# Kernel optimization log

Hardware: AMD Instinct MI355X
Metric: run time of the kernel (lower is better)

The kernel has to match this reference:

```python
import jax, jax.numpy as jnp
import numpy as np

B, L, C = 64, 2688, 256
W, S, H = 42, 21, 8   # window_size, shift_size, num_heads
HD = C // H
NW = L // W
MLP_H = 4 * C


def _layer_norm(v, g, b, eps=1e-5):
    m = v.mean(-1, keepdims=True)
    var = ((v - m) ** 2).mean(-1, keepdims=True)
    return (v - m) / jnp.sqrt(var + eps) * g + b


def setup_inputs() -> dict:
    key = jax.random.key(0)
    ks = jax.random.split(key, 8)
    std = 0.02
    return {
        "x": jax.random.normal(ks[0], (B, L, C), jnp.float32),
        "norm1_g": jnp.ones((C,), jnp.float32),
        "norm1_b": jnp.zeros((C,), jnp.float32),
        "qkv_w": jax.random.normal(ks[1], (C, 3 * C), jnp.float32) * std,
        "qkv_b": jnp.zeros((3 * C,), jnp.float32),
        "bias_table": jax.random.normal(ks[2], (2 * W - 1, H), jnp.float32) * std,
        "proj_w": jax.random.normal(ks[3], (C, C), jnp.float32) * std,
        "proj_b": jnp.zeros((C,), jnp.float32),
        "norm2_g": jnp.ones((C,), jnp.float32),
        "norm2_b": jnp.zeros((C,), jnp.float32),
        "fc1_w": jax.random.normal(ks[4], (C, MLP_H), jnp.float32) * std,
        "fc1_b": jnp.zeros((MLP_H,), jnp.float32),
        "fc2_w": jax.random.normal(ks[5], (MLP_H, C), jnp.float32) * std,
        "fc2_b": jnp.zeros((C,), jnp.float32),
    }


# ---- static (data-independent) index/mask tables ----
_rel_idx = np.arange(W)[None, :] - np.arange(W)[:, None] + W - 1  # (W, W)
_seg = np.zeros((L,), np.float32)
_seg[-W:-S] = 1.0
_seg[-S:] = 2.0
_mw = _seg.reshape(NW, W)
_am = _mw[:, None, :] - _mw[:, :, None]            # (nW, W, W)
_ATTN_MASK = np.where(_am != 0, -100.0, 0.0).astype(np.float32)


def reference(x, norm1_g, norm1_b, qkv_w, qkv_b, bias_table, proj_w, proj_b,
              norm2_g, norm2_b, fc1_w, fc1_b, fc2_w, fc2_b):
    mask = jnp.asarray(_ATTN_MASK)                  # (nW, W, W)
    scale = HD ** -0.5

    shortcut = x
    h = _layer_norm(x, norm1_g, norm1_b)
    h = jnp.roll(h, -S, axis=1)                     # cyclic shift
    xw = h.reshape(B * NW, W, C)                    # window partition

    qkv = (xw @ qkv_w + qkv_b).reshape(B * NW, W, 3, H, HD).transpose(2, 0, 3, 1, 4)
    q, k, v = qkv[0] * scale, qkv[1], qkv[2]        # each (B_, H, W, HD)
    attn = jnp.einsum('bhnd,bhmd->bhnm', q, k)      # (B_, H, W, W)

    rpb = bias_table[jnp.asarray(_rel_idx)]         # (W, W, H)
    attn = attn + rpb.transpose(2, 0, 1)[None]
    attn = attn.reshape(B, NW, H, W, W) + mask[None, :, None]
    attn = jax.nn.softmax(attn.reshape(B * NW, H, W, W), axis=-1)

    o = jnp.einsum('bhnm,bhmd->bhnd', attn, v)      # (B_, H, W, HD)
    o = o.transpose(0, 2, 1, 3).reshape(B * NW, W, C)
    o = o @ proj_w + proj_b

    h = jnp.roll(o.reshape(B, L, C), S, axis=1)     # reverse shift
    x1 = shortcut + h

    m = _layer_norm(x1, norm2_g, norm2_b)
    m = jax.nn.gelu(m @ fc1_w + fc1_b, approximate=False)
    m = m @ fc2_w + fc2_b
    return x1 + m
```

## Files before the change

### kernel.cpp

```cpp
#include <hip/hip_runtime.h>
#include <hip/hip_bf16.h>

typedef short short8 __attribute__((ext_vector_type(8)));
typedef float floatx4 __attribute__((ext_vector_type(4)));

constexpr int Bc = 64, Lc = 2688, Cc = 256, Wc = 42, Sc = 21;
constexpr int Mrows = Bc * Lc;
constexpr float QSCALE = 0.17677669529663689f;

#define GLOAD_LDS(g, l) __builtin_amdgcn_global_load_lds( \
    (const __attribute__((address_space(1))) void*)(g),   \
    (__attribute__((address_space(3))) void*)(l), 16, 0, 0)
#define BAR() __builtin_amdgcn_s_barrier()
#define WAITV4() asm volatile("s_waitcnt vmcnt(4)" ::: "memory")
#define WAITV0() asm volatile("s_waitcnt vmcnt(0)" ::: "memory")
#define LGKM0() do { asm volatile("s_waitcnt lgkmcnt(0)" ::: "memory"); \
                     __builtin_amdgcn_sched_barrier(0); } while (0)

__global__ __launch_bounds__(256) void transpose_cast_k(const float* __restrict__ w,
                                                        __hip_bfloat16* __restrict__ o,
                                                        int K, int N) {
  __shared__ float tile[32][33];
  int tx = threadIdx.x & 31, ty = threadIdx.x >> 5;
  int n0 = blockIdx.x * 32, k0 = blockIdx.y * 32;
#pragma unroll
  for (int r = 0; r < 32; r += 8)
    tile[ty + r][tx] = w[(size_t)(k0 + ty + r) * N + n0 + tx];
  __syncthreads();
#pragma unroll
  for (int r = 0; r < 32; r += 8)
    o[(size_t)(n0 + ty + r) * K + k0 + tx] = __float2bfloat16(tile[tx][ty + r]);
}

__global__ __launch_bounds__(256) void ln_k(const float* __restrict__ x, const float* __restrict__ g,
                                            const float* __restrict__ bta, __hip_bfloat16* __restrict__ out,
                                            int roll) {
  int row = blockIdx.x * 4 + (threadIdx.x >> 6);
  int lane = threadIdx.x & 63;
  int bb = row / Lc, rl = row - bb * Lc;
  int sl = rl + roll; if (sl >= Lc) sl -= Lc;
  const float4 v = *(const float4*)(x + ((size_t)bb * Lc + sl) * Cc + lane * 4);
  float s = v.x + v.y + v.z + v.w;
#pragma unroll
  for (int o = 1; o < 64; o <<= 1) s += __shfl_xor(s, o, 64);
  float mean = s * (1.0f / Cc);
  float d0 = v.x - mean, d1 = v.y - mean, d2 = v.z - mean, d3 = v.w - mean;
  float s2 = d0 * d0 + d1 * d1 + d2 * d2 + d3 * d3;
#pragma unroll
  for (int o = 1; o < 64; o <<= 1) s2 += __shfl_xor(s2, o, 64);
  float r = rsqrtf(s2 * (1.0f / Cc) + 1e-5f);
  const float4 gg = *(const float4*)(g + lane * 4);
  const float4 bb4 = *(const float4*)(bta + lane * 4);
  __hip_bfloat16 tmp[4];
  tmp[0] = __float2bfloat16(d0 * r * gg.x + bb4.x);
  tmp[1] = __float2bfloat16(d1 * r * gg.y + bb4.y);
  tmp[2] = __float2bfloat16(d2 * r * gg.z + bb4.z);
  tmp[3] = __float2bfloat16(d3 * r * gg.w + bb4.w);
  *(uint2*)(out + (size_t)row * Cc + lane * 4) = *(uint2*)tmp;
}

template <int EPI, int N, int K>
__global__ __launch_bounds__(512, 2) void gemm8(const __hip_bfloat16* __restrict__ A,
                                                const __hip_bfloat16* __restrict__ BT,
                                                const float* __restrict__ bias,
                                                const float* __restrict__ aux,
                                                void* __restrict__ outv) {
  constexpr int NT = K / 64;
  constexpr int NBX = N / 256;
  constexpr int NWG = NBX * (Mrows / 256);
  static_assert(NWG % 8 == 0, "xcd swizzle");
  __shared__ __align__(16) __hip_bfloat16 As[32768];
  __shared__ __align__(16) __hip_bfloat16 Bs[32768];

  const int t = threadIdx.x;
  const int wave = t >> 6, lane = t & 63, q = lane >> 4, lr = lane & 15;
  const int wm = (wave >> 2) * 128, wn = (wave & 3) * 64;

  const int orig = blockIdx.x;
  const int wgid = (orig & 7) * (NWG / 8) + (orig >> 3);
  const int bx = wgid % NBX, by = wgid / NBX;
  const int n0 = bx * 256, m0 = by * 256;

  auto srcoff = [&](int c) {
    int o = c * 16;
    int u = o ^ (((o >> 8) & 3) << 4);
    return (size_t)(u >> 6) * K + (size_t)((u >> 4) & 3) * 8;
  };
  const __hip_bfloat16* sA0 = A + (size_t)m0 * K + srcoff(t);
  const __hip_bfloat16* sA1 = A + (size_t)m0 * K + srcoff(512 + t);
  const __hip_bfloat16* sB0 = BT + (size_t)n0 * K + srcoff(t);
  const __hip_bfloat16* sB1 = BT + (size_t)n0 * K + srcoff(512 + t);

  int offA[8], offB[4];
#pragma unroll
  for (int i = 0; i < 8; i++) {
    int lin = (wm + i * 16 + lr) * 64 + q * 16;
    offA[i] = lin ^ (((lin >> 8) & 3) << 4);
  }
#pragma unroll
  for (int j = 0; j < 4; j++) {
    int lin = (wn + j * 16 + lr) * 64 + q * 16;
    offB[j] = lin ^ (((lin >> 8) & 3) << 4);
  }

  floatx4 acc[8][4] = {};
  short8 afr[4], bfr[4];

#define STAGE(s0, s1, region, koff) do {            \
    __hip_bfloat16* l_ = (region) + wave * 512;     \
    GLOAD_LDS((s0) + (koff), l_);                   \
    GLOAD_LDS((s1) + (koff), l_ + 4096); } while (0)

#define LDA4(base_, mq_) { \
    const char* Ab_ = (const char*)(base_); \
    _Pragma("unroll") for (int i_ = 0; i_ < 4; i_++) afr[i_] = *(const short8*)(Ab_ + offA[(mq_) * 4 + i_]); }
#define LDB4(base_) { \
    const char* Bb_ = (const char*)(base_); \
    _Pragma("unroll") for (int j_ = 0; j_ < 4; j_++) bfr[j_] = *(const short8*)(Bb_ + offB[j_]); }
#define MFMA16(mq_) \
    __builtin_amdgcn_s_setprio(1); \
    _Pragma("unroll") for (int i_ = 0; i_ < 4; i_++) \
    _Pragma("unroll") for (int j_ = 0; j_ < 4; j_++) \
      acc[(mq_) * 4 + i_][j_] = __builtin_amdgcn_mfma_f32_16x16x32_bf16(afr[i_], bfr[j_], acc[(mq_) * 4 + i_][j_], 0, 0, 0); \
    __builtin_amdgcn_s_setprio(0);

  STAGE(sA0, sA1, As + 0 * 8192, 0);
  STAGE(sB0, sB1, Bs + 0 * 8192, 0);
  STAGE(sA0, sA1, As + 1 * 8192, 32);
  STAGE(sB0, sB1, Bs + 1 * 8192, 32);
  WAITV0();
  BAR();

  for (int kt = 0; kt < NT - 1; ++kt) {
    const int buf = kt & 1, nbuf = buf ^ 1;
    const int kn = (kt + 1) * 64;
    __hip_bfloat16* A0 = As + (buf * 2 + 0) * 8192;
    __hip_bfloat16* A1 = As + (buf * 2 + 1) * 8192;
    __hip_bfloat16* B0 = Bs + (buf * 2 + 0) * 8192;
    __hip_bfloat16* B1 = Bs + (buf * 2 + 1) * 8192;
    LDA4(A0, 0); LDB4(B0);
    STAGE(sA0, sA1, As + (nbuf * 2 + 0) * 8192, kn);
    BAR(); LGKM0(); MFMA16(0); BAR();
    LDA4(A0, 1);
    STAGE(sB0, sB1, Bs + (nbuf * 2 + 0) * 8192, kn);
    BAR(); LGKM0(); MFMA16(1);
    WAITV4(); BAR();
    LDA4(A1, 0); LDB4(B1);
    STAGE(sA0, sA1, As + (nbuf * 2 + 1) * 8192, kn + 32);
    BAR(); LGKM0(); MFMA16(0); BAR();
    LDA4(A1, 1);
    STAGE(sB0, sB1, Bs + (nbuf * 2 + 1) * 8192, kn + 32);
    BAR(); LGKM0(); MFMA16(1);
    WAITV4(); BAR();
  }
  {
    const int buf = (NT - 1) & 1;
    __hip_bfloat16* A0 = As + (buf * 2 + 0) * 8192;
    __hip_bfloat16* A1 = As + (buf * 2 + 1) * 8192;
    __hip_bfloat16* B0 = Bs + (buf * 2 + 0) * 8192;
    __hip_bfloat16* B1 = Bs + (buf * 2 + 1) * 8192;
    LDA4(A0, 0); LDB4(B0);
    BAR(); LGKM0(); MFMA16(0); BAR();
    LDA4(A0, 1);
    BAR(); LGKM0(); MFMA16(1);
    WAITV0(); BAR();
    LDA4(A1, 0); LDB4(B1);
    BAR(); LGKM0(); MFMA16(0); BAR();
    LDA4(A1, 1);
    LGKM0(); MFMA16(1);
  }

  if (EPI == 0 || EPI == 2) {
    BAR();
    char* Tc = (char*)((wave < 4) ? (As + wave * 8192) : (Bs + (wave - 4) * 8192));
#pragma unroll
    for (int mf = 0; mf < 8; mf++) {
#pragma unroll
      for (int rg = 0; rg < 4; rg++) {
        int row = mf * 16 + q * 4 + rg;
        int sw = ((row >> 2) & 3) << 5;
#pragma unroll
        for (int nf = 0; nf < 4; nf++) {
          int lcol = nf * 16 + lr;
          int gcol = n0 + wn + lcol;
          float v = acc[mf][nf][rg] + bias[gcol];
          if (EPI == 0) {
            if (gcol < 256) v *= QSCALE;
          } else {
            float u = v * (0.7978845608028654f + 0.03567740813630012f * v * v);
            v = v * __builtin_amdgcn_rcpf(1.0f + __expf(-2.0f * u));
          }
          *(__hip_bfloat16*)(Tc + row * 128 + ((lcol * 2) ^ sw)) = __float2bfloat16(v);
        }
      }
    }
    LGKM0();
#pragma unroll
    for (int it = 0; it < 16; it++) {
      int id = it * 64 + lane;
      int row = id >> 3, cg = id & 7;
      short8 val = *(const short8*)(Tc + row * 128 + ((cg * 16) ^ (((row >> 2) & 3) << 5)));
      *(short8*)((__hip_bfloat16*)outv + (size_t)(m0 + wm + row) * N + (n0 + wn + cg * 8)) = val;
    }
  } else {
#pragma unroll
    for (int mf = 0; mf < 8; mf++) {
#pragma unroll
      for (int rg = 0; rg < 4; rg++) {
        int row = m0 + wm + mf * 16 + q * 4 + rg;
        int bb = 0, l = 0;
        if (EPI == 1) {
          bb = row / Lc;
          int rl = row - bb * Lc;
          l = rl + Sc; if (l >= Lc) l -= Lc;
        }
#pragma unroll
        for (int nf = 0; nf < 4; nf++) {
          int col = n0 + wn + nf * 16 + lr;
          float v = acc[mf][nf][rg] + bias[col];
          if (EPI == 1) {
            size_t o = ((size_t)bb * Lc + l) * Cc + col;
            ((float*)outv)[o] = aux[o] + v;
          } else {
            size_t o = (size_t)row * Cc + col;
            ((float*)outv)[o] = aux[o] + v;
          }
        }
      }
    }
  }
#undef STAGE
#undef LDA4
#undef LDB4
#undef MFMA16
}

constexpr int PSTR = 72;
constexpr int PSZ = 48 * PSTR;
constexpr int VTSZ = 32 * PSTR;

__global__ __launch_bounds__(256) void attn_k(const __hip_bfloat16* __restrict__ qkv,
                                              const float* __restrict__ bias_table,
                                              __hip_bfloat16* __restrict__ o_buf) {
  __shared__ __align__(16) __hip_bfloat16 smem[4 * PSZ + 4 * VTSZ];
  __shared__ float btab[83 * 8];
  const int t = threadIdx.x, wave = t >> 6, lane = t & 63, q = lane >> 4, lr = lane & 15;
  const int win = blockIdx.x >> 1;
  const int h = (blockIdx.x & 1) * 4 + wave;

  for (int i = t; i < (4 * PSZ + 4 * VTSZ) / 8; i += 256) ((uint4*)smem)[i] = uint4{0, 0, 0, 0};
  for (int i = t; i < 83 * 8; i += 256) btab[i] = bias_table[i];
  __syncthreads();

  __hip_bfloat16* Pw = smem + wave * PSZ;
  __hip_bfloat16* VTw = smem + 4 * PSZ + wave * VTSZ;
  const __hip_bfloat16* qbase = qkv + (size_t)win * 42 * 768 + h * 32;
  const __hip_bfloat16* kbase = qbase + 256;
  const __hip_bfloat16* vbase = qbase + 512;

  for (int c = lane; c < 42 * 4; c += 64) {
    int j = c >> 2, d0 = (c & 3) * 8;
    short8 vv = *(const short8*)(vbase + (size_t)j * 768 + d0);
#pragma unroll
    for (int e = 0; e < 8; e++) ((short*)VTw)[(d0 + e) * PSTR + j] = vv[e];
  }

  short8 qf[3], kf[3];
#pragma unroll
  for (int mt = 0; mt < 3; mt++) {
    int i = mt * 16 + lr; if (i > 41) i = 41;
    qf[mt] = *(const short8*)(qbase + (size_t)i * 768 + q * 8);
  }
#pragma unroll
  for (int nt = 0; nt < 3; nt++) {
    int j = nt * 16 + lr; if (j > 41) j = 41;
    kf[nt] = *(const short8*)(kbase + (size_t)j * 768 + q * 8);
  }
  floatx4 sacc[3][3] = {};
#pragma unroll
  for (int mt = 0; mt < 3; mt++)
#pragma unroll
    for (int nt = 0; nt < 3; nt++)
      sacc[mt][nt] = __builtin_amdgcn_mfma_f32_16x16x32_bf16(qf[mt], kf[nt], sacc[mt][nt], 0, 0, 0);

  const bool lastwin = ((win & 63) == 63);
#pragma unroll
  for (int mt = 0; mt < 3; mt++) {
#pragma unroll
    for (int rg = 0; rg < 4; rg++) {
      int row = mt * 16 + q * 4 + rg;
      float sv[3];
      float mx = -1e30f;
#pragma unroll
      for (int nt = 0; nt < 3; nt++) {
        int col = nt * 16 + lr;
        float s = sacc[mt][nt][rg];
        int ri = col - row + 41; ri = ri < 0 ? 0 : (ri > 82 ? 82 : ri);
        s += btab[ri * 8 + h];
        if (lastwin && ((row < 21) != (col < 21))) s -= 100.0f;
        if (col >= 42) s = -1e30f;
        sv[nt] = s;
        mx = fmaxf(mx, s);
      }
#pragma unroll
      for (int o = 1; o < 16; o <<= 1) mx = fmaxf(mx, __shfl_xor(mx, o, 64));
      float sum = 0.0f;
#pragma unroll
      for (int nt = 0; nt < 3; nt++) { float e = __expf(sv[nt] - mx); sv[nt] = e; sum += e; }
#pragma unroll
      for (int o = 1; o < 16; o <<= 1) sum += __shfl_xor(sum, o, 64);
      float inv = 1.0f / sum;
#pragma unroll
      for (int nt = 0; nt < 3; nt++) Pw[row * PSTR + nt * 16 + lr] = __float2bfloat16(sv[nt] * inv);
    }
  }
  __syncthreads();

  floatx4 oacc[3][2] = {};
#pragma unroll
  for (int ks = 0; ks < 2; ks++) {
    short8 pf[3], vf[2];
#pragma unroll
    for (int mt = 0; mt < 3; mt++) pf[mt] = *(const short8*)(Pw + (mt * 16 + lr) * PSTR + ks * 32 + q * 8);
#pragma unroll
    for (int nt = 0; nt < 2; nt++) vf[nt] = *(const short8*)(VTw + (nt * 16 + lr) * PSTR + ks * 32 + q * 8);
#pragma unroll
    for (int mt = 0; mt < 3; mt++)
#pragma unroll
      for (int nt = 0; nt < 2; nt++)
        oacc[mt][nt] = __builtin_amdgcn_mfma_f32_16x16x32_bf16(pf[mt], vf[nt], oacc[mt][nt], 0, 0, 0);
  }
#pragma unroll
  for (int mt = 0; mt < 3; mt++) {
#pragma unroll
    for (int rg = 0; rg < 4; rg++) {
      int row = mt * 16 + q * 4 + rg;
      if (row < 42) {
#pragma unroll
        for (int nt = 0; nt < 2; nt++) {
          int col = nt * 16 + lr;
          o_buf[((size_t)win * 42 + row) * 256 + h * 32 + col] = __float2bfloat16(oacc[mt][nt][rg]);
        }
      }
    }
  }
}

extern "C" void kernel_launch(void* const* d_in, const int* in_sizes, int n_in,
                              void* d_out, int out_size, void* d_ws, size_t ws_size,
                              hipStream_t stream) {
  const float* x       = (const float*)d_in[0];
  const float* norm1_g = (const float*)d_in[1];
  const float* norm1_b = (const float*)d_in[2];
  const float* qkv_w   = (const float*)d_in[3];
  const float* qkv_b   = (const float*)d_in[4];
  const float* btab    = (const float*)d_in[5];
  const float* proj_w  = (const float*)d_in[6];
  const float* proj_b  = (const float*)d_in[7];
  const float* norm2_g = (const float*)d_in[8];
  const float* norm2_b = (const float*)d_in[9];
  const float* fc1_w   = (const float*)d_in[10];
  const float* fc1_b   = (const float*)d_in[11];
  const float* fc2_w   = (const float*)d_in[12];
  const float* fc2_b   = (const float*)d_in[13];
  float* out = (float*)d_out;

  char* ws = (char*)d_ws;
  size_t off = 0;
  auto alloc = [&](size_t bytes) { char* p = ws + off; off += (bytes + 255) & ~(size_t)255; return p; };
  __hip_bfloat16* wT_qkv  = (__hip_bfloat16*)alloc((size_t)768 * 256 * 2);
  __hip_bfloat16* wT_proj = (__hip_bfloat16*)alloc((size_t)256 * 256 * 2);
  __hip_bfloat16* wT_fc1  = (__hip_bfloat16*)alloc((size_t)1024 * 256 * 2);
  __hip_bfloat16* wT_fc2  = (__hip_bfloat16*)alloc((size_t)256 * 1024 * 2);
  __hip_bfloat16* buf88   = (__hip_bfloat16*)alloc((size_t)Mrows * 256 * 2);
  __hip_bfloat16* buf352  = (__hip_bfloat16*)alloc((size_t)Mrows * 1024 * 2);

  transpose_cast_k<<<dim3(768 / 32, 256 / 32), 256, 0, stream>>>(qkv_w, wT_qkv, 256, 768);
  transpose_cast_k<<<dim3(256 / 32, 256 / 32), 256, 0, stream>>>(proj_w, wT_proj, 256, 256);
  transpose_cast_k<<<dim3(1024 / 32, 256 / 32), 256, 0, stream>>>(fc1_w, wT_fc1, 256, 1024);
  transpose_cast_k<<<dim3(256 / 32, 1024 / 32), 256, 0, stream>>>(fc2_w, wT_fc2, 1024, 256);

  ln_k<<<Mrows / 4, 256, 0, stream>>>(x, norm1_g, norm1_b, buf88, Sc);

  gemm8<0, 768, 256><<<dim3(3 * (Mrows / 256)), 512, 0, stream>>>(buf88, wT_qkv, qkv_b, nullptr, buf352);

  attn_k<<<(Mrows / Wc) * 2, 256, 0, stream>>>(buf352, btab, buf88);

  gemm8<1, 256, 256><<<dim3(Mrows / 256), 512, 0, stream>>>(buf88, wT_proj, proj_b, x, out);

  ln_k<<<Mrows / 4, 256, 0, stream>>>(out, norm2_g, norm2_b, buf88, 0);

  gemm8<2, 1024, 256><<<dim3(4 * (Mrows / 256)), 512, 0, stream>>>(buf88, wT_fc1, fc1_b, nullptr, buf352);

  gemm8<3, 256, 1024><<<dim3(Mrows / 256), 512, 0, stream>>>(buf352, wT_fc2, fc2_b, out, out);

  (void)in_sizes; (void)n_in; (void)out_size; (void)ws_size;
}
```

Measured before the change: 1.115 ms.

## Fuse LayerNorm2, fc1, GELU and fc2 into a single MLP kernel

Replaces the LayerNorm2 kernel and the two MLP GEMMs with one kernel. Each 128-row block normalizes its rows into LDS, computes fc1 in 256-column chunks with GELU into an LDS activation tile, and immediately accumulates fc2 on top of a residual-initialized accumulator. This removes the global round trip of the 1024-wide hidden activation and the normalized buffer. In exchange, B operands are read directly from global memory without LDS staging or software pipelining, and 128 KB of LDS per block limits occupancy, so the MFMA loops may be memory-latency bound.

```diff
diff --git a/kernel.cpp b/kernel.cpp
--- a/kernel.cpp
+++ b/kernel.cpp
@@ -170,7 +170,7 @@
     LGKM0(); MFMA16(1);
   }
 
-  if (EPI == 0 || EPI == 2) {
+  if (EPI == 0) {
     BAR();
     char* Tc = (char*)((wave < 4) ? (As + wave * 8192) : (Bs + (wave - 4) * 8192));
 #pragma unroll
@@ -184,12 +184,7 @@
           int lcol = nf * 16 + lr;
           int gcol = n0 + wn + lcol;
           float v = acc[mf][nf][rg] + bias[gcol];
-          if (EPI == 0) {
-            if (gcol < 256) v *= QSCALE;
-          } else {
-            float u = v * (0.7978845608028654f + 0.03567740813630012f * v * v);
-            v = v * __builtin_amdgcn_rcpf(1.0f + __expf(-2.0f * u));
-          }
+          if (gcol < 256) v *= QSCALE;
           *(__hip_bfloat16*)(Tc + row * 128 + ((lcol * 2) ^ sw)) = __float2bfloat16(v);
         }
       }
@@ -208,23 +203,15 @@
 #pragma unroll
       for (int rg = 0; rg < 4; rg++) {
         int row = m0 + wm + mf * 16 + q * 4 + rg;
-        int bb = 0, l = 0;
-        if (EPI == 1) {
-          bb = row / Lc;
-          int rl = row - bb * Lc;
-          l = rl + Sc; if (l >= Lc) l -= Lc;
-        }
+        int bb = row / Lc;
+        int rl = row - bb * Lc;
+        int l = rl + Sc; if (l >= Lc) l -= Lc;
 #pragma unroll
         for (int nf = 0; nf < 4; nf++) {
           int col = n0 + wn + nf * 16 + lr;
           float v = acc[mf][nf][rg] + bias[col];
-          if (EPI == 1) {
-            size_t o = ((size_t)bb * Lc + l) * Cc + col;
-            ((float*)outv)[o] = aux[o] + v;
-          } else {
-            size_t o = (size_t)row * Cc + col;
-            ((float*)outv)[o] = aux[o] + v;
-          }
+          size_t o = ((size_t)bb * Lc + l) * Cc + col;
+          ((float*)outv)[o] = aux[o] + v;
         }
       }
     }
@@ -233,6 +220,125 @@
 #undef LDA4
 #undef LDB4
 #undef MFMA16
+}
+
+__global__ __launch_bounds__(512, 2) void mlp_k(const float* __restrict__ x1,
+                                                const __hip_bfloat16* __restrict__ fc1T,
+                                                const float* __restrict__ b1,
+                                                const __hip_bfloat16* __restrict__ fc2T,
+                                                const float* __restrict__ b2,
+                                                const float* __restrict__ n2g,
+                                                const float* __restrict__ n2b,
+                                                float* __restrict__ out) {
+  __shared__ __align__(16) __hip_bfloat16 mA[128 * 256];
+  __shared__ __align__(16) __hip_bfloat16 act[128 * 256];
+  const int t = threadIdx.x, wave = t >> 6, lane = t & 63, q = lane >> 4, lr = lane & 15;
+  const int wm = (wave >> 2) * 64, wn = (wave & 3) * 64;
+  const int m0 = blockIdx.x * 128;
+
+  {
+    const float4 gg = *(const float4*)(n2g + lane * 4);
+    const float4 bv = *(const float4*)(n2b + lane * 4);
+#pragma unroll
+    for (int i = 0; i < 16; i++) {
+      int row = wave * 16 + i;
+      const float4 v = *(const float4*)(x1 + (size_t)(m0 + row) * 256 + lane * 4);
+      float s = v.x + v.y + v.z + v.w;
+#pragma unroll
+      for (int o = 1; o < 64; o <<= 1) s += __shfl_xor(s, o, 64);
+      float mean = s * (1.0f / 256.0f);
+      float d0 = v.x - mean, d1 = v.y - mean, d2 = v.z - mean, d3 = v.w - mean;
+      float s2 = d0 * d0 + d1 * d1 + d2 * d2 + d3 * d3;
+#pragma unroll
+      for (int o = 1; o < 64; o <<= 1) s2 += __shfl_xor(s2, o, 64);
+      float r = rsqrtf(s2 * (1.0f / 256.0f) + 1e-5f);
+      __hip_bfloat16 tmp[4];
+      tmp[0] = __float2bfloat16(d0 * r * gg.x + bv.x);
+      tmp[1] = __float2bfloat16(d1 * r * gg.y + bv.y);
+      tmp[2] = __float2bfloat16(d2 * r * gg.z + bv.z);
+      tmp[3] = __float2bfloat16(d3 * r * gg.w + bv.w);
+      *(uint2*)((char*)mA + row * 512 + ((lane * 8) ^ ((row & 7) << 4))) = *(uint2*)tmp;
+    }
+  }
+
+  floatx4 acc2[4][4];
+#pragma unroll
+  for (int mf = 0; mf < 4; mf++)
+#pragma unroll
+    for (int rg = 0; rg < 4; rg++) {
+      int row = m0 + wm + mf * 16 + q * 4 + rg;
+#pragma unroll
+      for (int nf = 0; nf < 4; nf++)
+        acc2[mf][nf][rg] = x1[(size_t)row * 256 + wn + nf * 16 + lr];
+    }
+  __syncthreads();
+
+  for (int c = 0; c < 4; c++) {
+    floatx4 acc1[4][4] = {};
+    const __hip_bfloat16* B1p = fc1T + (size_t)(c * 256) * 256;
+#pragma unroll
+    for (int ks = 0; ks < 8; ks++) {
+      short8 af[4], bf[4];
+#pragma unroll
+      for (int i = 0; i < 4; i++) {
+        int row = wm + i * 16 + lr;
+        af[i] = *(const short8*)((char*)mA + row * 512 + ((ks * 64 + q * 16) ^ ((row & 7) << 4)));
+      }
+#pragma unroll
+      for (int j = 0; j < 4; j++)
+        bf[j] = *(const short8*)(B1p + (size_t)(wn + j * 16 + lr) * 256 + ks * 32 + q * 8);
+#pragma unroll
+      for (int i = 0; i < 4; i++)
+#pragma unroll
+        for (int j = 0; j < 4; j++)
+          acc1[i][j] = __builtin_amdgcn_mfma_f32_16x16x32_bf16(af[i], bf[j], acc1[i][j], 0, 0, 0);
+    }
+    __syncthreads();
+#pragma unroll
+    for (int mf = 0; mf < 4; mf++)
+#pragma unroll
+      for (int rg = 0; rg < 4; rg++) {
+        int row = wm + mf * 16 + q * 4 + rg;
+#pragma unroll
+        for (int nf = 0; nf < 4; nf++) {
+          int col = wn + nf * 16 + lr;
+          float v = acc1[mf][nf][rg] + b1[c * 256 + col];
+          float u = v * (0.7978845608028654f + 0.03567740813630012f * v * v);
+          v = v * __builtin_amdgcn_rcpf(1.0f + __expf(-2.0f * u));
+          *(__hip_bfloat16*)((char*)act + row * 512 + ((col * 2) ^ ((row & 7) << 4))) = __float2bfloat16(v);
+        }
+      }
+    __syncthreads();
+#pragma unroll
+    for (int ks = 0; ks < 8; ks++) {
+      short8 af[4], bf[4];
+#pragma unroll
+      for (int i = 0; i < 4; i++) {
+        int row = wm + i * 16 + lr;
+        af[i] = *(const short8*)((char*)act + row * 512 + ((ks * 64 + q * 16) ^ ((row & 7) << 4)));
+      }
+#pragma unroll
+      for (int j = 0; j < 4; j++)
+        bf[j] = *(const short8*)(fc2T + (size_t)(wn + j * 16 + lr) * 1024 + c * 256 + ks * 32 + q * 8);
+#pragma unroll
+      for (int i = 0; i < 4; i++)
+#pragma unroll
+        for (int j = 0; j < 4; j++)
+          acc2[i][j] = __builtin_amdgcn_mfma_f32_16x16x32_bf16(af[i], bf[j], acc2[i][j], 0, 0, 0);
+    }
+  }
+
+#pragma unroll
+  for (int mf = 0; mf < 4; mf++)
+#pragma unroll
+    for (int rg = 0; rg < 4; rg++) {
+      int row = m0 + wm + mf * 16 + q * 4 + rg;
+#pragma unroll
+      for (int nf = 0; nf < 4; nf++) {
+        int col = wn + nf * 16 + lr;
+        out[(size_t)row * 256 + col] = acc2[mf][nf][rg] + b2[col];
+      }
+    }
 }
 
 constexpr int PSTR = 72;
@@ -388,11 +494,7 @@
 
   gemm8<1, 256, 256><<<dim3(Mrows / 256), 512, 0, stream>>>(buf88, wT_proj, proj_b, x, out);
 
-  ln_k<<<Mrows / 4, 256, 0, stream>>>(out, norm2_g, norm2_b, buf88, 0);
-
-  gemm8<2, 1024, 256><<<dim3(4 * (Mrows / 256)), 512, 0, stream>>>(buf88, wT_fc1, fc1_b, nullptr, buf352);
-
-  gemm8<3, 256, 1024><<<dim3(Mrows / 256), 512, 0, stream>>>(buf352, wT_fc2, fc2_b, out, out);
+  mlp_k<<<Mrows / 128, 512, 0, stream>>>(out, wT_fc1, fc1_b, wT_fc2, fc2_b, norm2_g, norm2_b, out);
 
   (void)in_sizes; (void)n_in; (void)out_size; (void)ws_size;
 }
```

After: 1.209 ms. 1.08x slower.
